# Optimization experiments

Measured on AMD Instinct MI355X. Metric: run time of the kernel, lower is better.

Reference implementation:

```python
import jax, jax.numpy as jnp
import numpy as np

B, S, D_IN, D_OUT, RANK = 4, 2048, 4096, 4096, 32
BLOCK = 16
Q_MAX = 7.0  # INT4: 2**(4-1) - 1


def quantize_uniform(x, block_size=BLOCK, q_max=Q_MAX):
    """Block-wise symmetric fake-quantize (round-to-nearest, clamp)."""
    orig_shape = x.shape
    xf = x.reshape(-1, block_size)
    amax = jnp.clip(jnp.max(jnp.abs(xf), axis=-1, keepdims=True), 1e-12, None)
    scale = amax / q_max
    xq = jnp.clip(jnp.round(xf / scale), -q_max, q_max) * scale
    return xq.reshape(orig_shape)


def setup_inputs() -> dict:
    key = jax.random.key(0)
    ks = jax.random.split(key, 7)
    x = jax.random.normal(ks[0], (B, S, D_IN), jnp.float32)
    smooth_scale = jax.random.uniform(ks[1], (D_IN,), jnp.float32, 0.5, 2.0)
    w_quantized = jax.random.normal(ks[2], (D_OUT, D_IN), jnp.float32) * 0.02
    lora_a = jax.random.normal(ks[3], (RANK, D_IN), jnp.float32) * 0.02
    lora_b = jax.random.normal(ks[4], (D_OUT, RANK), jnp.float32) * 0.02
    w_sparse = jax.random.normal(ks[5], (D_OUT, D_IN), jnp.float32) * 0.02
    bias = jax.random.normal(ks[6], (D_OUT,), jnp.float32) * 0.02
    return {"x": x, "smooth_scale": smooth_scale, "w_quantized": w_quantized,
            "lora_a": lora_a, "lora_b": lora_b, "w_sparse": w_sparse, "bias": bias}


def reference(x, smooth_scale, w_quantized, lora_a, lora_b, w_sparse, bias):
    # smoothing (SmoothQuant-style per-channel scale)
    x_smoothed = x * smooth_scale                      # [B,S,Din]
    # block-wise INT4 fake-quantize of the smoothed activations
    x_q = quantize_uniform(x_smoothed)                 # [B,S,Din]
    # quantized main path
    base_out = jnp.einsum('bsi,oi->bso', x_q, w_quantized)
    # low-rank SVD error-correction path
    svd_out = jnp.einsum('bsr,or->bso',
                         jnp.einsum('bsi,ri->bsr', x_smoothed, lora_a),
                         lora_b)
    # sparse-outlier path (unsmoothed x)
    sparse_out = jnp.einsum('bsi,oi->bso', x, w_sparse)
    return base_out + svd_out + sparse_out + bias
```

## Files before the change

kernel.cpp:

```cpp
#include <hip/hip_runtime.h>
#include <stdint.h>

typedef float  f32x4  __attribute__((ext_vector_type(4)));
typedef __bf16 bf16x8 __attribute__((ext_vector_type(8)));
typedef unsigned int   u32;
typedef unsigned short u16;
typedef unsigned long long u64;
typedef u32 u32x4 __attribute__((ext_vector_type(4)));

#define M_TOT 8192
#define N_TOT 4096
#define K_DIN 4096
#define RANK  32
#define KPAD  128
#define NTILE 130

__device__ __forceinline__ u16 f2bf(float f) {
  union { float f; u32 u; } v; v.f = f;
  u32 r = v.u + 0x7fffu + ((v.u >> 16) & 1u);
  return (u16)(r >> 16);
}

__global__ void prep_as_k(const float* __restrict__ la, const float* __restrict__ ss,
                          u16* __restrict__ asb) {
  int i = blockIdx.x * 256 + threadIdx.x;
  f32x4 v = ((const f32x4*)la)[i];
  f32x4 s = ((const f32x4*)ss)[i & 1023];
  f32x4 p = v * s;
  alignas(8) u16 o[4] = { f2bf(p[0]), f2bf(p[1]), f2bf(p[2]), f2bf(p[3]) };
  *(u64*)(asb + 4 * (size_t)i) = *(const u64*)o;
}

__global__ void cvt_bf16_k(const float* __restrict__ in, u16* __restrict__ out, int n4) {
  int i = blockIdx.x * 256 + threadIdx.x;
  if (i >= n4) return;
  f32x4 v = ((const f32x4*)in)[i];
  alignas(8) u16 o[4] = { f2bf(v[0]), f2bf(v[1]), f2bf(v[2]), f2bf(v[3]) };
  *(u64*)(out + 4 * (size_t)i) = *(const u64*)o;
}

__global__ void cvt_lb_k(const float* __restrict__ in, u16* __restrict__ out) {
  int i = blockIdx.x * 256 + threadIdx.x;
  f32x4 v = ((const f32x4*)in)[i];
  int row = i >> 3, c = (i & 7) * 4;
  alignas(8) u16 o[4] = { f2bf(v[0]), f2bf(v[1]), f2bf(v[2]), f2bf(v[3]) };
  *(u64*)(out + (size_t)row * KPAD + c) = *(const u64*)o;
}

__global__ void prep_x_k(const float* __restrict__ x, const float* __restrict__ ss,
                         u16* __restrict__ xq, u16* __restrict__ xb) {
  int m = blockIdx.x;
  int t = threadIdx.x;
  size_t off = (size_t)m * K_DIN + t * 16;
  const f32x4* xp = (const f32x4*)(x + off);
  const f32x4* sp = (const f32x4*)(ss + t * 16);
  float xs[16];
  alignas(16) u16 rb[16], qb[16];
  float amax = 0.0f;
  #pragma unroll
  for (int i = 0; i < 4; ++i) {
    f32x4 a = xp[i], s = sp[i];
    #pragma unroll
    for (int j = 0; j < 4; ++j) {
      float xr = a[j];
      float v  = xr * s[j];
      xs[i*4+j] = v;
      amax = fmaxf(amax, fabsf(v));
      rb[i*4+j] = f2bf(xr);
    }
  }
  amax = fmaxf(amax, 1e-12f);
  float scale = amax / 7.0f;
  #pragma unroll
  for (int i = 0; i < 16; ++i) {
    float r = rintf(xs[i] / scale);
    r = fminf(7.0f, fmaxf(-7.0f, r));
    qb[i] = f2bf(r * scale);
  }
  ((u32x4*)(xq + off))[0] = ((const u32x4*)qb)[0];
  ((u32x4*)(xq + off))[1] = ((const u32x4*)qb)[1];
  ((u32x4*)(xb + off))[0] = ((const u32x4*)rb)[0];
  ((u32x4*)(xb + off))[1] = ((const u32x4*)rb)[1];
}

__global__ __launch_bounds__(256)
void lora_t_mfma_k(const u16* __restrict__ xb, const u16* __restrict__ asb,
                   u16* __restrict__ tb) {
  const int wave = threadIdx.x >> 6;
  const int lane = threadIdx.x & 63;
  const int lr = lane & 15, lg = lane >> 4;
  const int m0 = blockIdx.x * 64 + wave * 16;
  f32x4 acc0 = {}, acc1 = {};
  for (int k0 = 0; k0 < K_DIN; k0 += 32) {
    bf16x8 a  = *(const bf16x8*)(xb  + (size_t)(m0 + lr) * K_DIN + k0 + lg * 8);
    bf16x8 b0 = *(const bf16x8*)(asb + (size_t)lr        * K_DIN + k0 + lg * 8);
    bf16x8 b1 = *(const bf16x8*)(asb + (size_t)(16 + lr) * K_DIN + k0 + lg * 8);
    acc0 = __builtin_amdgcn_mfma_f32_16x16x32_bf16(a, b0, acc0, 0, 0, 0);
    acc1 = __builtin_amdgcn_mfma_f32_16x16x32_bf16(a, b1, acc1, 0, 0, 0);
  }
  #pragma unroll
  for (int j = 0; j < 4; ++j) {
    const int row = m0 + lg * 4 + j;
    tb[(size_t)row * KPAD + lr]      = f2bf(acc0[j]);
    tb[(size_t)row * KPAD + 16 + lr] = f2bf(acc1[j]);
  }
}

__device__ __forceinline__ void gld_lds16(const u16* g, u16* l) {
  __builtin_amdgcn_global_load_lds((const __attribute__((address_space(1))) u32*)g,
                                   (__attribute__((address_space(3))) u32*)l,
                                   16, 0, 0);
}

#define BAR()  asm volatile("s_barrier" ::: "memory")
#define VMW4() asm volatile("s_waitcnt vmcnt(4)" ::: "memory")

#define LDA(bufel, mh) do { _Pragma("unroll")                                        \
  for (int m_ = 0; m_ < 4; ++m_) {                                                   \
    Ar[m_][0] = *(const bf16x8*)(smem + (bufel) + aoff + ((mh)*4+m_)*1024 + blk0);    \
    Ar[m_][1] = *(const bf16x8*)(smem + (bufel) + aoff + ((mh)*4+m_)*1024 + blk1);    \
  } } while (0)

#define LDB(bufel, nh) do { _Pragma("unroll")                                        \
  for (int n_ = 0; n_ < 2; ++n_) {                                                   \
    Br[(nh)*2+n_][0] = *(const bf16x8*)(smem + (bufel) + boff + ((nh)*2+n_)*1024 + blk0); \
    Br[(nh)*2+n_][1] = *(const bf16x8*)(smem + (bufel) + boff + ((nh)*2+n_)*1024 + blk1); \
  } } while (0)

#define MMQ(mh, nh) do {                                                             \
  __builtin_amdgcn_s_setprio(1);                                                     \
  _Pragma("unroll")                                                                  \
  for (int m_ = 0; m_ < 4; ++m_) { _Pragma("unroll")                                 \
    for (int n_ = 0; n_ < 2; ++n_) {                                                 \
      acc[(mh)*4+m_][(nh)*2+n_] = __builtin_amdgcn_mfma_f32_16x16x32_bf16(           \
          Ar[m_][0], Br[(nh)*2+n_][0], acc[(mh)*4+m_][(nh)*2+n_], 0, 0, 0);          \
      acc[(mh)*4+m_][(nh)*2+n_] = __builtin_amdgcn_mfma_f32_16x16x32_bf16(           \
          Ar[m_][1], Br[(nh)*2+n_][1], acc[(mh)*4+m_][(nh)*2+n_], 0, 0, 0);          \
    } }                                                                              \
  __builtin_amdgcn_s_setprio(0);                                                     \
} while (0)

__global__ __launch_bounds__(512, 2)
void gemm8_k(const u16* __restrict__ xq, const u16* __restrict__ xb,
             const u16* __restrict__ tb, const u16* __restrict__ wqb,
             const u16* __restrict__ wsb, const u16* __restrict__ lbp,
             const float* __restrict__ bias, float* __restrict__ out) {
  extern __shared__ u16 smem[];
  const int tid  = threadIdx.x;
  const int wave = tid >> 6;
  const int lane = tid & 63;
  const int lr = lane & 15, lg = lane >> 4;
  const int wm = wave >> 2, wn = wave & 3;

  const int wg  = blockIdx.x;
  const int swz = (wg & 7) * 64 + (wg >> 3);
  const int m0 = (swz >> 4) * 256;
  const int n0 = (swz & 15) * 256;

  const int aoff = wm * 8192 + lr * 64;
  const int boff = 16384 + wn * 4096 + lr * 64;
  const int e7   = lr & 7;
  const int blk0 = ((0 + lg) ^ e7) * 8;
  const int blk1 = ((4 + lg) ^ e7) * 8;

  const int srow = tid >> 3;
  const int scol = ((tid & 7) ^ (srow & 7)) * 8;
  const int woff = wave * 512;

  bf16x8 Ar[4][2], Br[4][2];
  f32x4 acc[8][4] = {};

  auto stage = [&](int tt, int mat, int h, int bufel) {
    if (tt > NTILE - 1) tt = NTILE - 1;
    const u16* p; size_t stride; int kof;
    if (tt < 64)       { p = mat ? wqb : xq; stride = 4096; kof = tt * 64; }
    else if (tt < 128) { p = mat ? wsb : xb; stride = 4096; kof = (tt - 64) * 64; }
    else               { p = mat ? lbp : tb; stride = KPAD; kof = (tt - 128) * 64; }
    const int rb = (mat ? n0 : m0) + h * 128 + srow;
    u16* dst = smem + bufel + mat * 16384 + h * 8192 + woff;
    gld_lds16(p + (size_t)rb * stride + kof + scol, dst);
    gld_lds16(p + (size_t)(rb + 64) * stride + kof + scol, dst + 4096);
  };

  stage(0, 0, 0, 0);     stage(0, 0, 1, 0);
  stage(0, 1, 0, 0);     stage(0, 1, 1, 0);
  stage(1, 1, 0, 32768); stage(1, 1, 1, 32768);
  VMW4();
  BAR();

  for (int it = 0; it < NTILE / 2; ++it) {
    const int a = 2 * it;
    LDA(0, 0); LDB(0, 0);
    stage(a + 1, 0, 0, 32768);
    BAR(); MMQ(0, 0); BAR();
    LDB(0, 1);
    stage(a + 1, 0, 1, 32768);
    BAR(); MMQ(0, 1); BAR();
    LDA(0, 1);
    stage(a + 2, 1, 0, 0);
    BAR(); MMQ(1, 1); BAR();
    stage(a + 2, 1, 1, 0);
    VMW4();
    BAR(); MMQ(1, 0); BAR();
    LDA(32768, 0); LDB(32768, 0);
    stage(a + 2, 0, 0, 0);
    BAR(); MMQ(0, 0); BAR();
    LDB(32768, 1);
    stage(a + 2, 0, 1, 0);
    BAR(); MMQ(0, 1); BAR();
    LDA(32768, 1);
    stage(a + 3, 1, 0, 32768);
    BAR(); MMQ(1, 1); BAR();
    stage(a + 3, 1, 1, 32768);
    VMW4();
    BAR(); MMQ(1, 0); BAR();
  }

  float bv[4];
  #pragma unroll
  for (int n = 0; n < 4; ++n) bv[n] = bias[n0 + wn * 64 + n * 16 + lr];
  #pragma unroll
  for (int m = 0; m < 8; ++m) {
    const int row = m0 + wm * 128 + m * 16 + lg * 4;
    #pragma unroll
    for (int n = 0; n < 4; ++n) {
      const int col = n0 + wn * 64 + n * 16 + lr;
      float* op = out + (size_t)row * N_TOT + col;
      op[0 * (size_t)N_TOT] = acc[m][n][0] + bv[n];
      op[1 * (size_t)N_TOT] = acc[m][n][1] + bv[n];
      op[2 * (size_t)N_TOT] = acc[m][n][2] + bv[n];
      op[3 * (size_t)N_TOT] = acc[m][n][3] + bv[n];
    }
  }
}

extern "C" void kernel_launch(void* const* d_in, const int* in_sizes, int n_in,
                              void* d_out, int out_size, void* d_ws, size_t ws_size,
                              hipStream_t stream) {
  const float* x    = (const float*)d_in[0];
  const float* ss   = (const float*)d_in[1];
  const float* wq   = (const float*)d_in[2];
  const float* la   = (const float*)d_in[3];
  const float* lb   = (const float*)d_in[4];
  const float* wsp  = (const float*)d_in[5];
  const float* bias = (const float*)d_in[6];
  float* out = (float*)d_out;

  uint8_t* w = (uint8_t*)d_ws;
  u16* xq   = (u16*)w;  w += (size_t)M_TOT * K_DIN * 2;
  u16* xb   = (u16*)w;  w += (size_t)M_TOT * K_DIN * 2;
  u16* wqb  = (u16*)w;  w += (size_t)N_TOT * K_DIN * 2;
  u16* wsb  = (u16*)w;  w += (size_t)N_TOT * K_DIN * 2;
  u16* tb   = (u16*)w;  w += (size_t)M_TOT * KPAD * 2;
  u16* lbp  = (u16*)w;  w += (size_t)N_TOT * KPAD * 2;
  u16* asb  = (u16*)w;

  hipMemsetAsync(tb, 0, ((size_t)M_TOT + N_TOT) * KPAD * 2, stream);
  prep_as_k<<<128, 256, 0, stream>>>(la, ss, asb);
  cvt_bf16_k<<<16384, 256, 0, stream>>>(wq,  wqb, (N_TOT * K_DIN) / 4);
  cvt_bf16_k<<<16384, 256, 0, stream>>>(wsp, wsb, (N_TOT * K_DIN) / 4);
  cvt_lb_k<<<128, 256, 0, stream>>>(lb, lbp);
  prep_x_k<<<M_TOT, 256, 0, stream>>>(x, ss, xq, xb);
  lora_t_mfma_k<<<M_TOT / 64, 256, 0, stream>>>(xb, asb, tb);

  hipFuncSetAttribute((const void*)gemm8_k,
                      hipFuncAttributeMaxDynamicSharedMemorySize, 131072);
  gemm8_k<<<dim3((N_TOT / 256) * (M_TOT / 256)), 512, 131072, stream>>>(
      xq, xb, tb, wqb, wsb, lbp, bias, out);
}
```

Measured before the change: 602.8 us.

## Reschedule GEMM load/compute pipeline with deeper prefetch and scheduler-fenced barriers

Reorders the global-to-LDS stage calls so the next tile's A-half is issued one phase earlier, and relaxes the wait from vmcnt(4) to vmcnt(6) so more loads stay in flight. Barriers become builtin s_barrier wrapped in sched_barrier fences, which stop the compiler from moving instructions across them. The aim is better overlap of memory latency with MFMA work. The new stage ordering and vmcnt counts must still protect every buffer before it is read; an error there would produce a race.

```diff
diff --git a/kernel.cpp b/kernel.cpp
--- a/kernel.cpp
+++ b/kernel.cpp
@@ -112,8 +112,12 @@
                                    16, 0, 0);
 }
 
-#define BAR()  asm volatile("s_barrier" ::: "memory")
-#define VMW4() asm volatile("s_waitcnt vmcnt(4)" ::: "memory")
+#define BARX() do { __builtin_amdgcn_sched_barrier(0);                               \
+                    __builtin_amdgcn_s_barrier();                                    \
+                    __builtin_amdgcn_sched_barrier(0); } while (0)
+#define VMW6() asm volatile("s_waitcnt vmcnt(6)" ::: "memory")
+
+#define BUF1 32768
 
 #define LDA(bufel, mh) do { _Pragma("unroll")                                        \
   for (int m_ = 0; m_ < 4; ++m_) {                                                   \
@@ -184,36 +188,39 @@
 
   stage(0, 0, 0, 0);     stage(0, 0, 1, 0);
   stage(0, 1, 0, 0);     stage(0, 1, 1, 0);
-  stage(1, 1, 0, 32768); stage(1, 1, 1, 32768);
-  VMW4();
-  BAR();
+  stage(1, 1, 0, BUF1);  stage(1, 1, 1, BUF1);
+  stage(1, 0, 0, BUF1);
+  VMW6();
+  BARX();
 
   for (int it = 0; it < NTILE / 2; ++it) {
     const int a = 2 * it;
     LDA(0, 0); LDB(0, 0);
-    stage(a + 1, 0, 0, 32768);
-    BAR(); MMQ(0, 0); BAR();
+    stage(a + 1, 0, 1, BUF1);
+    BARX(); MMQ(0, 0); BARX();
     LDB(0, 1);
-    stage(a + 1, 0, 1, 32768);
-    BAR(); MMQ(0, 1); BAR();
+    BARX(); MMQ(0, 1); BARX();
     LDA(0, 1);
     stage(a + 2, 1, 0, 0);
-    BAR(); MMQ(1, 1); BAR();
     stage(a + 2, 1, 1, 0);
-    VMW4();
-    BAR(); MMQ(1, 0); BAR();
-    LDA(32768, 0); LDB(32768, 0);
+    BARX(); MMQ(1, 1); BARX();
     stage(a + 2, 0, 0, 0);
-    BAR(); MMQ(0, 0); BAR();
-    LDB(32768, 1);
+    BARX(); MMQ(1, 0);
+    VMW6();
+    BARX();
+    LDA(BUF1, 0); LDB(BUF1, 0);
     stage(a + 2, 0, 1, 0);
-    BAR(); MMQ(0, 1); BAR();
-    LDA(32768, 1);
-    stage(a + 3, 1, 0, 32768);
-    BAR(); MMQ(1, 1); BAR();
-    stage(a + 3, 1, 1, 32768);
-    VMW4();
-    BAR(); MMQ(1, 0); BAR();
+    BARX(); MMQ(0, 0); BARX();
+    LDB(BUF1, 1);
+    BARX(); MMQ(0, 1); BARX();
+    LDA(BUF1, 1);
+    stage(a + 3, 1, 0, BUF1);
+    stage(a + 3, 1, 1, BUF1);
+    BARX(); MMQ(1, 1); BARX();
+    stage(a + 3, 0, 0, BUF1);
+    BARX(); MMQ(1, 0);
+    VMW6();
+    BARX();
   }
 
   float bv[4];
```

Measured after the change: 608.3 us. About the same (+0.9%).

## Concatenate GEMM operands into single K-concatenated A/B buffers and reschedule staging

Applied to the files above, without the earlier changes.

Packs quantized x, raw x and the LoRA intermediate into one row-major A buffer of width 8320, and the two weight matrices plus LoRA B into one matching B buffer. The GEMM then stages from a single base pointer per operand with a plain k offset instead of branching per tile. The separate memset is replaced by explicit zeroing of the padding columns. The prefetch schedule is reordered so each half-iteration issues more loads ahead, and the wait moves from vmcnt(4) to vmcnt(6). The barrier now uses the compiler builtin rather than inline asm.

```diff
diff --git a/kernel.cpp b/kernel.cpp
--- a/kernel.cpp
+++ b/kernel.cpp
@@ -12,7 +12,7 @@
 #define N_TOT 4096
 #define K_DIN 4096
 #define RANK  32
-#define KPAD  128
+#define KCAT  8320
 #define NTILE 130
 
 __device__ __forceinline__ u16 f2bf(float f) {
@@ -31,28 +31,30 @@
   *(u64*)(asb + 4 * (size_t)i) = *(const u64*)o;
 }
 
-__global__ void cvt_bf16_k(const float* __restrict__ in, u16* __restrict__ out, int n4) {
+__global__ void cvt_w_k(const float* __restrict__ in, u16* __restrict__ Bb, int colofs) {
   int i = blockIdx.x * 256 + threadIdx.x;
-  if (i >= n4) return;
   f32x4 v = ((const f32x4*)in)[i];
+  int r = i >> 10, c = (i & 1023) * 4;
   alignas(8) u16 o[4] = { f2bf(v[0]), f2bf(v[1]), f2bf(v[2]), f2bf(v[3]) };
-  *(u64*)(out + 4 * (size_t)i) = *(const u64*)o;
-}
-
-__global__ void cvt_lb_k(const float* __restrict__ in, u16* __restrict__ out) {
+  *(u64*)(Bb + (size_t)r * KCAT + colofs + c) = *(const u64*)o;
+}
+
+__global__ void cvt_lb_k(const float* __restrict__ in, u16* __restrict__ Bb) {
   int i = blockIdx.x * 256 + threadIdx.x;
   f32x4 v = ((const f32x4*)in)[i];
   int row = i >> 3, c = (i & 7) * 4;
   alignas(8) u16 o[4] = { f2bf(v[0]), f2bf(v[1]), f2bf(v[2]), f2bf(v[3]) };
-  *(u64*)(out + (size_t)row * KPAD + c) = *(const u64*)o;
+  u16* rp = Bb + (size_t)row * KCAT;
+  *(u64*)(rp + 2 * K_DIN + c) = *(const u64*)o;
+  u16* zp = rp + 2 * K_DIN + RANK + (i & 7) * 12;
+  *(u64*)(zp + 0) = 0; *(u64*)(zp + 4) = 0; *(u64*)(zp + 8) = 0;
 }
 
 __global__ void prep_x_k(const float* __restrict__ x, const float* __restrict__ ss,
-                         u16* __restrict__ xq, u16* __restrict__ xb) {
+                         u16* __restrict__ Ab) {
   int m = blockIdx.x;
   int t = threadIdx.x;
-  size_t off = (size_t)m * K_DIN + t * 16;
-  const f32x4* xp = (const f32x4*)(x + off);
+  const f32x4* xp = (const f32x4*)(x + (size_t)m * K_DIN + t * 16);
   const f32x4* sp = (const f32x4*)(ss + t * 16);
   float xs[16];
   alignas(16) u16 rb[16], qb[16];
@@ -77,22 +79,23 @@
     r = fminf(7.0f, fmaxf(-7.0f, r));
     qb[i] = f2bf(r * scale);
   }
-  ((u32x4*)(xq + off))[0] = ((const u32x4*)qb)[0];
-  ((u32x4*)(xq + off))[1] = ((const u32x4*)qb)[1];
-  ((u32x4*)(xb + off))[0] = ((const u32x4*)rb)[0];
-  ((u32x4*)(xb + off))[1] = ((const u32x4*)rb)[1];
+  u16* qo = Ab + (size_t)m * KCAT + t * 16;
+  ((u32x4*)qo)[0] = ((const u32x4*)qb)[0];
+  ((u32x4*)qo)[1] = ((const u32x4*)qb)[1];
+  u16* ro = qo + K_DIN;
+  ((u32x4*)ro)[0] = ((const u32x4*)rb)[0];
+  ((u32x4*)ro)[1] = ((const u32x4*)rb)[1];
 }
 
 __global__ __launch_bounds__(256)
-void lora_t_mfma_k(const u16* __restrict__ xb, const u16* __restrict__ asb,
-                   u16* __restrict__ tb) {
+void lora_t_mfma_k(u16* __restrict__ Ab, const u16* __restrict__ asb) {
   const int wave = threadIdx.x >> 6;
   const int lane = threadIdx.x & 63;
   const int lr = lane & 15, lg = lane >> 4;
   const int m0 = blockIdx.x * 64 + wave * 16;
   f32x4 acc0 = {}, acc1 = {};
   for (int k0 = 0; k0 < K_DIN; k0 += 32) {
-    bf16x8 a  = *(const bf16x8*)(xb  + (size_t)(m0 + lr) * K_DIN + k0 + lg * 8);
+    bf16x8 a  = *(const bf16x8*)(Ab + (size_t)(m0 + lr) * KCAT + K_DIN + k0 + lg * 8);
     bf16x8 b0 = *(const bf16x8*)(asb + (size_t)lr        * K_DIN + k0 + lg * 8);
     bf16x8 b1 = *(const bf16x8*)(asb + (size_t)(16 + lr) * K_DIN + k0 + lg * 8);
     acc0 = __builtin_amdgcn_mfma_f32_16x16x32_bf16(a, b0, acc0, 0, 0, 0);
@@ -101,9 +104,13 @@
   #pragma unroll
   for (int j = 0; j < 4; ++j) {
     const int row = m0 + lg * 4 + j;
-    tb[(size_t)row * KPAD + lr]      = f2bf(acc0[j]);
-    tb[(size_t)row * KPAD + 16 + lr] = f2bf(acc1[j]);
-  }
+    Ab[(size_t)row * KCAT + 2 * K_DIN + lr]      = f2bf(acc0[j]);
+    Ab[(size_t)row * KCAT + 2 * K_DIN + 16 + lr] = f2bf(acc1[j]);
+  }
+  const int zr = blockIdx.x * 64 + (threadIdx.x >> 2);
+  u16* zp = Ab + (size_t)zr * KCAT + 2 * K_DIN + RANK + (threadIdx.x & 3) * 24;
+  #pragma unroll
+  for (int q = 0; q < 6; ++q) *(u64*)(zp + q * 4) = 0;
 }
 
 __device__ __forceinline__ void gld_lds16(const u16* g, u16* l) {
@@ -112,8 +119,9 @@
                                    16, 0, 0);
 }
 
-#define BAR()  asm volatile("s_barrier" ::: "memory")
-#define VMW4() asm volatile("s_waitcnt vmcnt(4)" ::: "memory")
+#define BAR()  __builtin_amdgcn_s_barrier()
+#define VMW6() asm volatile("s_waitcnt vmcnt(6)" ::: "memory")
+#define BUF1 32768
 
 #define LDA(bufel, mh) do { _Pragma("unroll")                                        \
   for (int m_ = 0; m_ < 4; ++m_) {                                                   \
@@ -141,9 +149,7 @@
 } while (0)
 
 __global__ __launch_bounds__(512, 2)
-void gemm8_k(const u16* __restrict__ xq, const u16* __restrict__ xb,
-             const u16* __restrict__ tb, const u16* __restrict__ wqb,
-             const u16* __restrict__ wsb, const u16* __restrict__ lbp,
+void gemm8_k(const u16* __restrict__ Ab, const u16* __restrict__ Bb,
              const float* __restrict__ bias, float* __restrict__ out) {
   extern __shared__ u16 smem[];
   const int tid  = threadIdx.x;
@@ -167,53 +173,61 @@
   const int scol = ((tid & 7) ^ (srow & 7)) * 8;
   const int woff = wave * 512;
 
+  const u16* aRow = Ab + (size_t)(m0 + srow) * KCAT + scol;
+  const u16* bRow = Bb + (size_t)(n0 + srow) * KCAT + scol;
+  u16* dstA0 = smem + woff;
+  u16* dstB0 = smem + 16384 + woff;
+
   bf16x8 Ar[4][2], Br[4][2];
   f32x4 acc[8][4] = {};
 
-  auto stage = [&](int tt, int mat, int h, int bufel) {
-    if (tt > NTILE - 1) tt = NTILE - 1;
-    const u16* p; size_t stride; int kof;
-    if (tt < 64)       { p = mat ? wqb : xq; stride = 4096; kof = tt * 64; }
-    else if (tt < 128) { p = mat ? wsb : xb; stride = 4096; kof = (tt - 64) * 64; }
-    else               { p = mat ? lbp : tb; stride = KPAD; kof = (tt - 128) * 64; }
-    const int rb = (mat ? n0 : m0) + h * 128 + srow;
-    u16* dst = smem + bufel + mat * 16384 + h * 8192 + woff;
-    gld_lds16(p + (size_t)rb * stride + kof + scol, dst);
-    gld_lds16(p + (size_t)(rb + 64) * stride + kof + scol, dst + 4096);
+  auto stgA = [&](int kof, int h, int bufel) {
+    u16* dst = dstA0 + bufel + h * 8192;
+    gld_lds16(aRow + (size_t)(h * 128) * KCAT + kof, dst);
+    gld_lds16(aRow + (size_t)(h * 128 + 64) * KCAT + kof, dst + 4096);
   };
-
-  stage(0, 0, 0, 0);     stage(0, 0, 1, 0);
-  stage(0, 1, 0, 0);     stage(0, 1, 1, 0);
-  stage(1, 1, 0, 32768); stage(1, 1, 1, 32768);
-  VMW4();
+  auto stgB = [&](int kof, int h, int bufel) {
+    u16* dst = dstB0 + bufel + h * 8192;
+    gld_lds16(bRow + (size_t)(h * 128) * KCAT + kof, dst);
+    gld_lds16(bRow + (size_t)(h * 128 + 64) * KCAT + kof, dst + 4096);
+  };
+
+  stgA(0, 0, 0);     stgA(0, 1, 0);
+  stgB(0, 0, 0);     stgB(0, 1, 0);
+  stgB(64, 0, BUF1); stgB(64, 1, BUF1);
+  stgA(64, 0, BUF1);
+  VMW6();
   BAR();
 
   for (int it = 0; it < NTILE / 2; ++it) {
-    const int a = 2 * it;
+    const int ka = it * 128;
+    int c2 = ka + 128, c3 = ka + 192;
+    if (c2 > (NTILE - 1) * 64) c2 = (NTILE - 1) * 64;
+    if (c3 > (NTILE - 1) * 64) c3 = (NTILE - 1) * 64;
     LDA(0, 0); LDB(0, 0);
-    stage(a + 1, 0, 0, 32768);
+    stgA(ka + 64, 1, BUF1);
     BAR(); MMQ(0, 0); BAR();
     LDB(0, 1);
-    stage(a + 1, 0, 1, 32768);
     BAR(); MMQ(0, 1); BAR();
     LDA(0, 1);
-    stage(a + 2, 1, 0, 0);
+    stgB(c2, 0, 0); stgB(c2, 1, 0);
     BAR(); MMQ(1, 1); BAR();
-    stage(a + 2, 1, 1, 0);
-    VMW4();
-    BAR(); MMQ(1, 0); BAR();
-    LDA(32768, 0); LDB(32768, 0);
-    stage(a + 2, 0, 0, 0);
+    stgA(c2, 0, 0);
+    BAR(); MMQ(1, 0);
+    VMW6();
+    BAR();
+    LDA(BUF1, 0); LDB(BUF1, 0);
+    stgA(c2, 1, 0);
     BAR(); MMQ(0, 0); BAR();
-    LDB(32768, 1);
-    stage(a + 2, 0, 1, 0);
+    LDB(BUF1, 1);
     BAR(); MMQ(0, 1); BAR();
-    LDA(32768, 1);
-    stage(a + 3, 1, 0, 32768);
+    LDA(BUF1, 1);
+    stgB(c3, 0, BUF1); stgB(c3, 1, BUF1);
     BAR(); MMQ(1, 1); BAR();
-    stage(a + 3, 1, 1, 32768);
-    VMW4();
-    BAR(); MMQ(1, 0); BAR();
+    stgA(c3, 0, BUF1);
+    BAR(); MMQ(1, 0);
+    VMW6();
+    BAR();
   }
 
   float bv[4];
@@ -247,24 +261,19 @@
   float* out = (float*)d_out;
 
   uint8_t* w = (uint8_t*)d_ws;
-  u16* xq   = (u16*)w;  w += (size_t)M_TOT * K_DIN * 2;
-  u16* xb   = (u16*)w;  w += (size_t)M_TOT * K_DIN * 2;
-  u16* wqb  = (u16*)w;  w += (size_t)N_TOT * K_DIN * 2;
-  u16* wsb  = (u16*)w;  w += (size_t)N_TOT * K_DIN * 2;
-  u16* tb   = (u16*)w;  w += (size_t)M_TOT * KPAD * 2;
-  u16* lbp  = (u16*)w;  w += (size_t)N_TOT * KPAD * 2;
-  u16* asb  = (u16*)w;
-
-  hipMemsetAsync(tb, 0, ((size_t)M_TOT + N_TOT) * KPAD * 2, stream);
+  u16* Ab  = (u16*)w;  w += (size_t)M_TOT * KCAT * 2;
+  u16* Bb  = (u16*)w;  w += (size_t)N_TOT * KCAT * 2;
+  u16* asb = (u16*)w;
+
   prep_as_k<<<128, 256, 0, stream>>>(la, ss, asb);
-  cvt_bf16_k<<<16384, 256, 0, stream>>>(wq,  wqb, (N_TOT * K_DIN) / 4);
-  cvt_bf16_k<<<16384, 256, 0, stream>>>(wsp, wsb, (N_TOT * K_DIN) / 4);
-  cvt_lb_k<<<128, 256, 0, stream>>>(lb, lbp);
-  prep_x_k<<<M_TOT, 256, 0, stream>>>(x, ss, xq, xb);
-  lora_t_mfma_k<<<M_TOT / 64, 256, 0, stream>>>(xb, asb, tb);
+  cvt_w_k<<<16384, 256, 0, stream>>>(wq,  Bb, 0);
+  cvt_w_k<<<16384, 256, 0, stream>>>(wsp, Bb, K_DIN);
+  cvt_lb_k<<<128, 256, 0, stream>>>(lb, Bb);
+  prep_x_k<<<M_TOT, 256, 0, stream>>>(x, ss, Ab);
+  lora_t_mfma_k<<<M_TOT / 64, 256, 0, stream>>>(Ab, asb);
 
   hipFuncSetAttribute((const void*)gemm8_k,
                       hipFuncAttributeMaxDynamicSharedMemorySize, 131072);
   gemm8_k<<<dim3((N_TOT / 256) * (M_TOT / 256)), 512, 131072, stream>>>(
-      xq, xb, tb, wqb, wsb, lbp, bias, out);
-}
+      Ab, Bb, bias, out);
+}
```

New measurement: 595.7 us. About the same (-1.2%).
